# Kernel tuning notes

Measured on AMD Instinct MI355X. Metric: run time of the kernel, lower is better.

## Reference

```python
import jax, jax.numpy as jnp
import numpy as np

DIM = 1024
HEADS = 16
D_HEAD = 64
INNER = HEADS * D_HEAD  # 1024
FF_INNER = 4 * DIM      # 4096


def setup_inputs() -> dict:
    key = jax.random.key(0)
    ks = jax.random.split(key, 12)
    s = lambda fan_in: 1.0 / np.sqrt(fan_in)
    x = jax.random.normal(ks[0], (4, 1024, DIM), dtype=jnp.float32)
    context = jax.random.normal(ks[1], (4, 2048, DIM), dtype=jnp.float32)
    Wq = jax.random.normal(ks[2], (DIM, INNER), dtype=jnp.float32) * s(DIM)
    Wk = jax.random.normal(ks[3], (DIM, INNER), dtype=jnp.float32) * s(DIM)
    Wv = jax.random.normal(ks[4], (DIM, INNER), dtype=jnp.float32) * s(DIM)
    Wo = jax.random.normal(ks[5], (INNER, DIM), dtype=jnp.float32) * s(INNER)
    bo = jax.random.normal(ks[6], (DIM,), dtype=jnp.float32) * 0.01
    W1 = jax.random.normal(ks[7], (DIM, FF_INNER), dtype=jnp.float32) * s(DIM)
    b1 = jax.random.normal(ks[8], (FF_INNER,), dtype=jnp.float32) * 0.01
    W2 = jax.random.normal(ks[9], (FF_INNER, DIM), dtype=jnp.float32) * s(FF_INNER)
    b2 = jax.random.normal(ks[10], (DIM,), dtype=jnp.float32) * 0.01
    return {"x": x, "context": context, "Wq": Wq, "Wk": Wk, "Wv": Wv,
            "Wo": Wo, "bo": bo, "W1": W1, "b1": b1, "W2": W2, "b2": b2}


def _block(x, context, Wq, Wk, Wv, Wo, bo, W1, b1, W2, b2):
    B, Lq, _ = x.shape
    scale = 1.0 / np.sqrt(D_HEAD).astype(np.float32)
    # cross attention
    q = (x @ Wq).reshape(B, Lq, HEADS, D_HEAD)          # [B,Lq,H,D]
    k = (context @ Wk).reshape(B, -1, HEADS, D_HEAD)    # [B,Lk,H,D]
    v = (context @ Wv).reshape(B, -1, HEADS, D_HEAD)
    sim = jnp.einsum('bqhd,bkhd->bhqk', q, k) * scale   # [B,H,Lq,Lk]
    attn = jax.nn.softmax(sim, axis=-1)
    out = jnp.einsum('bhqk,bkhd->bqhd', attn, v).reshape(B, Lq, INNER)
    x = out @ Wo + bo + x
    # feedforward (exact GELU as in torch F.gelu default)
    h = jax.nn.gelu(x @ W1 + b1, approximate=False)
    return h @ W2 + b2 + x


def reference(x, context, Wq, Wk, Wv, Wo, bo, W1, b1, W2, b2):
    return _block(x, context, Wq, Wk, Wv, Wo, bo, W1, b1, W2, b2)
```

## Files before the change

kernel.cpp:

```cpp
#include <hip/hip_runtime.h>
#include <hip/hip_bf16.h>
#include <cmath>
#include <cstdint>

typedef short s16x8 __attribute__((ext_vector_type(8)));
typedef unsigned short u16x8 __attribute__((ext_vector_type(8)));
typedef unsigned short u16x4 __attribute__((ext_vector_type(4)));
typedef float f32x4 __attribute__((ext_vector_type(4)));

__device__ __forceinline__ float bf2f(uint16_t u) {
  union { uint32_t i; float f; } c; c.i = ((uint32_t)u) << 16; return c.f;
}
__device__ __forceinline__ uint16_t f2bf(float f) {
  union { float f; uint32_t i; } c; c.f = f;
  return (uint16_t)((c.i + 0x7FFFu + ((c.i >> 16) & 1u)) >> 16);
}
__device__ __forceinline__ uint32_t pkbf(float a, float b) {
  union { __hip_bfloat162 h; uint32_t u; } c;
  c.h = __float22bfloat162_rn(float2{a, b});
  return c.u;
}

__device__ __forceinline__ void gload16(const void* g, void* l) {
  __builtin_amdgcn_global_load_lds(
      (const __attribute__((address_space(1))) void*)g,
      (__attribute__((address_space(3))) void*)l, 16, 0, 0);
}

__device__ __forceinline__ bool sniff_is_bf16(const uint16_t* u16, int64_t n,
                                              int tid, int* s_cnt) {
  int cnt = 0;
#pragma unroll
  for (int j = 0; j < 4; j++) {
    int64_t idx = (((int64_t)(tid * 4 + j)) * 2) % n;
    idx &= ~(int64_t)1;
    uint32_t e = (u16[idx] >> 7) & 0xFF;
    cnt += (e >= 96 && e <= 144) ? 1 : 0;
  }
  if (tid == 0) *s_cnt = 0;
  __syncthreads();
  atomicAdd(s_cnt, cnt);
  __syncthreads();
  return (*s_cnt) * 10 > 1024 * 6;
}

__global__ __launch_bounds__(256) void prep_all(
    float* dout,
    const void* xr, const void* cr, const void* bor, const void* b1r, const void* b2r,
    const void* Wq, const void* Wk, const void* Wv, const void* Wo,
    const void* W1, const void* W2,
    uint16_t* xo, uint16_t* co, uint16_t* boo, uint16_t* b1o, uint16_t* b2o,
    uint16_t* WqT, uint16_t* WkT, uint16_t* WvT, uint16_t* WoT,
    uint16_t* W1T, uint16_t* W2T) {
  __shared__ int s_cnt;
  __shared__ uint16_t tile[64][65];
  const int id = blockIdx.x;
  const int tid = threadIdx.x;

  if (id < 1024) {
    float* p = dout + ((int64_t)id * 256 + tid) * 4;
#pragma unroll
    for (int i = 0; i < 4; i++)
      *(f32x4*)(p + (int64_t)i * 262144) = (f32x4){0.f, 0.f, 0.f, 0.f};
    return;
  }
  if (id < 4099) {
    const void* src; uint16_t* dst; int64_t tot; int64_t base; int nv;
    if (id < 2048)      { src = xr; dst = xo; tot = 4194304; base = (int64_t)(id - 1024) * 4096; nv = 4; }
    else if (id < 4096) { src = cr; dst = co; tot = 8388608; base = (int64_t)(id - 2048) * 4096; nv = 4; }
    else if (id == 4096){ src = bor; dst = boo; tot = 1024; base = 0; nv = 1; }
    else if (id == 4097){ src = b1r; dst = b1o; tot = 4096; base = 0; nv = 4; }
    else                { src = b2r; dst = b2o; tot = 1024; base = 0; nv = 1; }
    const bool is16 = sniff_is_bf16((const uint16_t*)src, tot, tid, &s_cnt);
    if (is16) {
      const uint64_t* s = (const uint64_t*)((const uint16_t*)src + base);
      uint64_t* d = (uint64_t*)(dst + base);
      for (int i = 0; i < nv; i++) d[i * 256 + tid] = s[i * 256 + tid];
    } else {
      const f32x4* s = (const f32x4*)((const float*)src + base);
      uint2* d = (uint2*)(dst + base);
      for (int i = 0; i < nv; i++) {
        f32x4 v = s[i * 256 + tid];
        uint2 o; o.x = pkbf(v[0], v[1]); o.y = pkbf(v[2], v[3]);
        d[i * 256 + tid] = o;
      }
    }
    return;
  }
  const int t0 = id - 4099;
  const void* src; uint16_t* dst; int R, C, bx, by;
  if (t0 < 1024) {
    const int wsel = t0 >> 8, t = t0 & 255;
    const void* srcs[4] = {Wq, Wk, Wv, Wo};
    uint16_t* dsts[4] = {WqT, WkT, WvT, WoT};
    src = srcs[wsel]; dst = dsts[wsel]; R = 1024; C = 1024; bx = t & 15; by = t >> 4;
  } else if (t0 < 2048) { int t = t0 - 1024; src = W1; dst = W1T; R = 1024; C = 4096; bx = t & 63; by = t >> 6; }
  else                  { int t = t0 - 2048; src = W2; dst = W2T; R = 4096; C = 1024; bx = t & 15; by = t >> 4; }
  const uint16_t* u16 = (const uint16_t*)src;
  const float* f32 = (const float*)src;
  const bool is16 = sniff_is_bf16(u16, (int64_t)R * C, tid, &s_cnt);
  const int c0 = bx * 64, r0 = by * 64;
  if (is16) {
    const int c8 = (tid & 7) * 8, r = tid >> 3;
#pragma unroll
    for (int ri = 0; ri < 2; ri++) {
      const int row = r + ri * 32;
      u16x8 v = *(const u16x8*)(u16 + (int64_t)(r0 + row) * C + c0 + c8);
#pragma unroll
      for (int j = 0; j < 8; j++) tile[c8 + j][row] = v[j];
    }
  } else {
    const int c4 = (tid & 15) * 4, r = tid >> 4;
#pragma unroll
    for (int ri = 0; ri < 4; ri++) {
      const int row = r + ri * 16;
      f32x4 v = *(const f32x4*)(f32 + (int64_t)(r0 + row) * C + c0 + c4);
#pragma unroll
      for (int j = 0; j < 4; j++) tile[c4 + j][row] = f2bf(v[j]);
    }
  }
  __syncthreads();
  const int rr8 = (tid & 7) * 8, cc = tid >> 3;
#pragma unroll
  for (int ci = 0; ci < 2; ci++) {
    const int col = cc + ci * 32;
    *(u16x8*)(dst + (int64_t)(c0 + col) * R + r0 + rr8) = *(const u16x8*)&tile[col][rr8];
  }
}

__global__ __launch_bounds__(256) void vtrans(
    const uint16_t* __restrict__ KVb, uint16_t* __restrict__ Vt) {
  __shared__ uint16_t tile[64][65];
  const int z = blockIdx.z;
  const uint16_t* in = KVb + (int64_t)z * 2048 * 2048 + 1024;
  uint16_t* out = Vt + (int64_t)z * 1024 * 2048;
  const int tid = threadIdx.x;
  const int c0 = blockIdx.x * 64, k0 = blockIdx.y * 64;
  const int c8 = (tid & 7) * 8, r = tid >> 3;
#pragma unroll
  for (int ri = 0; ri < 2; ri++) {
    const int krow = r + ri * 32;
    u16x8 v = *(const u16x8*)(in + (int64_t)(k0 + krow) * 2048 + c0 + c8);
#pragma unroll
    for (int j = 0; j < 8; j++) tile[c8 + j][krow] = v[j];
  }
  __syncthreads();
  const int k8 = (tid & 7) * 8, cc = tid >> 3;
#pragma unroll
  for (int ci = 0; ci < 2; ci++) {
    const int col = cc + ci * 32;
    *(u16x8*)(out + (int64_t)(c0 + col) * 2048 + k0 + k8) = *(const u16x8*)&tile[col][k8];
  }
}

#define BM 128
#define BN 128
#define BK 64

enum { EPI_NONE = 0, EPI_BIAS_RES = 1, EPI_BIAS_GELU = 2 };

template <int EPI, int RESF32, int OUTF32, int SPLITK>
__device__ __forceinline__ void gemm_body(
    const uint16_t* __restrict__ A, const uint16_t* __restrict__ Bt,
    void* __restrict__ Cv, const uint16_t* __restrict__ bias,
    const void* __restrict__ resid, int M, int N, int K_total,
    int m0, int n0, int zslice, uint16_t* As, uint16_t* Bs) {
  const int tid = threadIdx.x;
  const int w = tid >> 6, l = tid & 63;
  const int wu = __builtin_amdgcn_readfirstlane(w);
  const int wm = (w >> 1) * 64, wn = (w & 1) * 64;
  const int ls = l & 15, lg = l >> 4;
  const int K = SPLITK ? (K_total >> 1) : K_total;
  const int kof = SPLITK ? zslice * K : 0;

  const int sr = 8 * w + (l >> 3);
  const int koff = (((l & 7) ^ ((l >> 3) & 7)) * 8);
  const uint16_t* Ag = A + (int64_t)(m0 + sr) * K_total + kof + koff;
  const uint16_t* Bg = Bt + (int64_t)(n0 + sr) * K_total + kof + koff;
  const int64_t rstep = (int64_t)32 * K_total;

  uint16_t* lA = As + wu * 512;
  uint16_t* lB = Bs + wu * 512;

  f32x4 acc[4][4] = {};

  for (int kb = 0; kb < K; kb += BK) {
    __syncthreads();
#pragma unroll
    for (int r = 0; r < 4; r++) {
      gload16(Ag + r * rstep + kb, lA + r * 2048);
      gload16(Bg + r * rstep + kb, lB + r * 2048);
    }
    __syncthreads();
#pragma unroll
    for (int kk = 0; kk < 2; kk++) {
      s16x8 af[4], bfr[4];
#pragma unroll
      for (int i = 0; i < 4; i++) {
        const int row = wm + i * 16 + ls;
        af[i] = *(const s16x8*)&As[row * 64 + (((kk * 4 + lg) ^ (ls & 7)) * 8)];
      }
#pragma unroll
      for (int j = 0; j < 4; j++) {
        const int row = wn + j * 16 + ls;
        bfr[j] = *(const s16x8*)&Bs[row * 64 + (((kk * 4 + lg) ^ (ls & 7)) * 8)];
      }
#pragma unroll
      for (int i = 0; i < 4; i++)
#pragma unroll
        for (int j = 0; j < 4; j++)
          acc[i][j] = __builtin_amdgcn_mfma_f32_16x16x32_bf16(af[i], bfr[j], acc[i][j], 0, 0, 0);
    }
  }

#pragma unroll
  for (int i = 0; i < 4; i++) {
#pragma unroll
    for (int rr = 0; rr < 4; rr++) {
      const int64_t row = m0 + wm + i * 16 + lg * 4 + rr;
#pragma unroll
      for (int j = 0; j < 4; j++) {
        const int col = n0 + wn + j * 16 + ls;
        float v = acc[i][j][rr];
        if (EPI == EPI_BIAS_RES) {
          if (!SPLITK || zslice == 0) {
            const float rv = RESF32 ? ((const float*)resid)[row * N + col]
                                    : bf2f(((const uint16_t*)resid)[row * N + col]);
            v += bf2f(bias[col]) + rv;
          }
        } else if (EPI == EPI_BIAS_GELU) {
          v += bf2f(bias[col]);
          v = 0.5f * v * (1.0f + erff(v * 0.70710678118654752f));
        }
        if (SPLITK)
          atomicAdd((float*)Cv + row * N + col, v);
        else if (OUTF32)
          ((float*)Cv)[row * N + col] = v;
        else
          ((uint16_t*)Cv)[row * N + col] = f2bf(v);
      }
    }
  }
}

template <int EPI, int RESF32, int OUTF32, int SPLITK>
__global__ __launch_bounds__(256, 3) void gemm_single(
    const uint16_t* __restrict__ A, const uint16_t* __restrict__ Bt,
    void* __restrict__ Cv, const uint16_t* __restrict__ bias,
    const void* __restrict__ resid, int M, int N, int K_total) {
  __shared__ alignas(16) uint16_t As[BM * BK];
  __shared__ alignas(16) uint16_t Bs[BN * BK];
  gemm_body<EPI, RESF32, OUTF32, SPLITK>(A, Bt, Cv, bias, resid, M, N, K_total,
                                         blockIdx.x * BM, blockIdx.y * BN,
                                         (int)blockIdx.z, As, Bs);
}

__global__ __launch_bounds__(256, 3) void gemm_qkv(
    const uint16_t* __restrict__ xA, const uint16_t* __restrict__ WqT,
    uint16_t* __restrict__ Qb,
    const uint16_t* __restrict__ ctxA, const uint16_t* __restrict__ KVWt,
    uint16_t* __restrict__ KVb) {
  __shared__ alignas(16) uint16_t As[BM * BK];
  __shared__ alignas(16) uint16_t Bs[BN * BK];
  const int id = blockIdx.x;
  if (id < 256) {
    gemm_body<EPI_NONE, 0, 0, 0>(xA, WqT, Qb, nullptr, nullptr, 4096, 1024, 1024,
                                 (id & 31) * BM, (id >> 5) * BN, 0, As, Bs);
  } else {
    const int t = id - 256;
    gemm_body<EPI_NONE, 0, 0, 0>(ctxA, KVWt, KVb, nullptr, nullptr, 8192, 2048, 1024,
                                 (t & 63) * BM, (t >> 6) * BN, 0, As, Bs);
  }
}

#define KLD 72
#define PLD 72

__global__ __launch_bounds__(256, 2) void attn_kernel(
    const uint16_t* __restrict__ Q,
    const uint16_t* __restrict__ KV,
    const uint16_t* __restrict__ Vt,
    uint16_t* __restrict__ O) {
  __shared__ alignas(16) uint16_t Ks[64 * KLD];
  __shared__ alignas(16) uint16_t Vts[64 * KLD];
  __shared__ alignas(16) uint16_t Ps[8][16 * PLD];

  const int tid = threadIdx.x;
  const int w = tid >> 6, l = tid & 63;
  const int ls = l & 15, lg = l >> 4;

  const int blk = blockIdx.x;
  const int bh = blk & 63;
  const int qb = blk >> 6;
  const int h = bh & 15, b = bh >> 4;

  const int64_t qrow0 = (int64_t)b * 1024 + qb * 128;
  const int hoff = h * 64;
  const uint16_t* Vtb = Vt + (int64_t)b * 1024 * 2048;

  const float sc = 0.125f * 1.4426950408889634f;

  s16x8 qf[2][2];
#pragma unroll
  for (int qq = 0; qq < 2; qq++)
#pragma unroll
    for (int ks = 0; ks < 2; ks++) {
      s16x8 r = *(const s16x8*)(Q + (qrow0 + w * 32 + qq * 16 + ls) * 1024 + hoff + ks * 32 + lg * 8);
#pragma unroll
      for (int j = 0; j < 8; j++)
        qf[qq][ks][j] = (short)f2bf(bf2f((uint16_t)r[j]) * sc);
    }

  f32x4 oacc[2][4] = {};
  float lsum[2] = {0.f, 0.f};

  const int srow = tid >> 3;
  const int sc8 = (tid & 7) * 8;
  const uint16_t* Kg = KV + ((int64_t)b * 2048 + srow) * 2048 + hoff + sc8;
  const uint16_t* Vg = Vtb + (int64_t)(hoff + srow) * 2048 + sc8;

  s16x8 rk0 = *(const s16x8*)(Kg);
  s16x8 rk1 = *(const s16x8*)(Kg + (int64_t)32 * 2048);
  s16x8 rv0 = *(const s16x8*)(Vg);
  s16x8 rv1 = *(const s16x8*)(Vg + (int64_t)32 * 2048);

  for (int kt = 0; kt < 2048; kt += 64) {
    __syncthreads();
    *(s16x8*)&Ks[srow * KLD + sc8] = rk0;
    *(s16x8*)&Ks[(srow + 32) * KLD + sc8] = rk1;
    *(s16x8*)&Vts[srow * KLD + sc8] = rv0;
    *(s16x8*)&Vts[(srow + 32) * KLD + sc8] = rv1;
    const int ktn = kt + 64;
    if (ktn < 2048) {
      rk0 = *(const s16x8*)(Kg + (int64_t)ktn * 2048);
      rk1 = *(const s16x8*)(Kg + (int64_t)(ktn + 32) * 2048);
      rv0 = *(const s16x8*)(Vg + ktn);
      rv1 = *(const s16x8*)(Vg + ktn + (int64_t)32 * 2048);
    }
    __syncthreads();

    f32x4 st[2][4];
#pragma unroll
    for (int jn = 0; jn < 4; jn++) {
      f32x4 z = {0.f, 0.f, 0.f, 0.f};
      st[0][jn] = z; st[1][jn] = z;
#pragma unroll
      for (int ks = 0; ks < 2; ks++) {
        s16x8 kf = *(const s16x8*)&Ks[(jn * 16 + ls) * KLD + ks * 32 + lg * 8];
        st[0][jn] = __builtin_amdgcn_mfma_f32_16x16x32_bf16(kf, qf[0][ks], st[0][jn], 0, 0, 0);
        st[1][jn] = __builtin_amdgcn_mfma_f32_16x16x32_bf16(kf, qf[1][ks], st[1][jn], 0, 0, 0);
      }
    }

#pragma unroll
    for (int qq = 0; qq < 2; qq++)
#pragma unroll
      for (int jn = 0; jn < 4; jn++) {
        const float p0 = exp2f(st[qq][jn][0]);
        const float p1 = exp2f(st[qq][jn][1]);
        const float p2 = exp2f(st[qq][jn][2]);
        const float p3 = exp2f(st[qq][jn][3]);
        lsum[qq] += (p0 + p1) + (p2 + p3);
        uint2 pk; pk.x = pkbf(p0, p1); pk.y = pkbf(p2, p3);
        *(uint2*)&Ps[w * 2 + qq][ls * PLD + jn * 16 + lg * 4] = pk;
      }

#pragma unroll
    for (int ks = 0; ks < 2; ks++) {
      s16x8 pf0 = *(const s16x8*)&Ps[w * 2 + 0][ls * PLD + ks * 32 + lg * 8];
      s16x8 pf1 = *(const s16x8*)&Ps[w * 2 + 1][ls * PLD + ks * 32 + lg * 8];
#pragma unroll
      for (int jn = 0; jn < 4; jn++) {
        s16x8 vf = *(const s16x8*)&Vts[(jn * 16 + ls) * KLD + ks * 32 + lg * 8];
        oacc[0][jn] = __builtin_amdgcn_mfma_f32_16x16x32_bf16(pf0, vf, oacc[0][jn], 0, 0, 0);
        oacc[1][jn] = __builtin_amdgcn_mfma_f32_16x16x32_bf16(pf1, vf, oacc[1][jn], 0, 0, 0);
      }
    }
  }

#pragma unroll
  for (int qq = 0; qq < 2; qq++) {
    float red = lsum[qq];
    red += __shfl_xor(red, 16, 64);
    red += __shfl_xor(red, 32, 64);
#pragma unroll
    for (int rr = 0; rr < 4; rr++) {
      const float inv = 1.0f / __shfl(red, lg * 4 + rr, 64);
      const int64_t row = qrow0 + w * 32 + qq * 16 + lg * 4 + rr;
#pragma unroll
      for (int jn = 0; jn < 4; jn++)
        O[row * 1024 + hoff + jn * 16 + ls] = f2bf(oacc[qq][jn][rr] * inv);
    }
  }
}

extern "C" void kernel_launch(void* const* d_in, const int* in_sizes, int n_in,
                              void* d_out, int out_size, void* d_ws, size_t ws_size,
                              hipStream_t stream) {
  const void* x_raw   = d_in[0];
  const void* ctx_raw = d_in[1];
  const void* Wq_raw  = d_in[2];
  const void* Wk_raw  = d_in[3];
  const void* Wv_raw  = d_in[4];
  const void* Wo_raw  = d_in[5];
  const void* bo_raw  = d_in[6];
  const void* W1_raw  = d_in[7];
  const void* b1_raw  = d_in[8];
  const void* W2_raw  = d_in[9];
  const void* b2_raw  = d_in[10];

  const int64_t Mi = 1 << 20;
  uint16_t* ws   = (uint16_t*)d_ws;
  uint16_t* WqT  = ws;
  uint16_t* KVWt = ws + 1 * Mi;
  uint16_t* WoT  = ws + 3 * Mi;
  uint16_t* W1T  = ws + 4 * Mi;
  uint16_t* W2T  = ws + 8 * Mi;
  uint16_t* bob  = ws + 12 * Mi;
  uint16_t* b1b  = ws + 12 * Mi + 1024;
  uint16_t* b2b  = ws + 12 * Mi + 5120;
  uint16_t* xb   = ws + 13 * Mi;
  uint16_t* AO   = ws + 13 * Mi;
  uint16_t* ctxb = ws + 17 * Mi;
  uint16_t* Vt   = ws + 17 * Mi;
  uint16_t* X1   = ws + 17 * Mi;
  uint16_t* Qb   = ws + 25 * Mi;
  uint16_t* KVb  = ws + 29 * Mi;
  uint16_t* Hb   = ws + 29 * Mi;

  const dim3 tb(256);
  prep_all<<<dim3(7171), tb, 0, stream>>>(
      (float*)d_out,
      x_raw, ctx_raw, bo_raw, b1_raw, b2_raw,
      Wq_raw, Wk_raw, Wv_raw, Wo_raw, W1_raw, W2_raw,
      xb, ctxb, bob, b1b, b2b,
      WqT, KVWt, KVWt + Mi, WoT, W1T, W2T);

  gemm_qkv<<<dim3(1280), tb, 0, stream>>>(xb, WqT, Qb, ctxb, KVWt, KVb);

  vtrans<<<dim3(16, 32, 4), tb, 0, stream>>>(KVb, Vt);

  attn_kernel<<<dim3(512), tb, 0, stream>>>(Qb, KVb, Vt, AO);

  gemm_single<EPI_BIAS_RES, 1, 0, 0><<<dim3(32, 8), tb, 0, stream>>>(
      AO, WoT, X1, bob, x_raw, 4096, 1024, 1024);
  gemm_single<EPI_BIAS_GELU, 0, 0, 0><<<dim3(32, 32), tb, 0, stream>>>(
      X1, W1T, Hb, b1b, nullptr, 4096, 4096, 1024);
  gemm_single<EPI_BIAS_RES, 0, 1, 1><<<dim3(32, 8, 2), tb, 0, stream>>>(
      Hb, W2T, d_out, b2b, X1, 4096, 1024, 4096);
}
```

Before: 400.8 us.

## Add 256x256 eight-wave double-buffered GEMM with phased LDS prefetch for QKV and FFN

Adds a new GEMM kernel that uses 512 threads and 256x256 output tiles. It double-buffers LDS and interleaves global-to-LDS prefetch of the next K-tile with four MFMA phases, using barriers, waitcnt and setprio. The kernel is used for the fused QKV projection, the W1+GELU GEMM, and the W2 GEMM, which now uses 4-way split-K with atomics. Larger tiles raise operand reuse and cut global traffic. The trade-off is fewer blocks: 320, 256 and 256 respectively, which may underfill 256 CUs and unbalance the QKV launch. The 4-way split-K also adds atomic contention.

```diff
diff --git a/kernel.cpp b/kernel.cpp
--- a/kernel.cpp
+++ b/kernel.cpp
@@ -153,11 +153,11 @@
   }
 }
 
+enum { EPI_NONE = 0, EPI_BIAS_RES = 1, EPI_BIAS_GELU = 2 };
+
 #define BM 128
 #define BN 128
 #define BK 64
-
-enum { EPI_NONE = 0, EPI_BIAS_RES = 1, EPI_BIAS_GELU = 2 };
 
 template <int EPI, int RESF32, int OUTF32, int SPLITK>
 __device__ __forceinline__ void gemm_body(
@@ -255,21 +255,140 @@
                                          (int)blockIdx.z, As, Bs);
 }
 
-__global__ __launch_bounds__(256, 3) void gemm_qkv(
+#define G8K 64
+
+#define STAGE_A8(BB, Q, KB) \
+  gload16(Ag + (int64_t)(Q) * cstep + (KB), As + (BB) + (Q) * 4096 + wu * 512)
+#define STAGE_B8(BB, Q, KB) \
+  gload16(Bg + (int64_t)(Q) * cstep + (KB), Bs + (BB) + (Q) * 4096 + wu * 512)
+
+#define PHASE8(QM, QN, S0, S1, WAITC)                                          \
+  do {                                                                         \
+    s16x8 a0_[4], a1_[4], b0_[2], b1_[2];                                      \
+    const int x_ = (ls & 7);                                                   \
+    _Pragma("unroll") for (int i_ = 0; i_ < 4; i_++) {                         \
+      const int r_ = wm + (QM) * 64 + i_ * 16 + ls;                            \
+      a0_[i_] = *(const s16x8*)&As[cb + r_ * 64 + ((lg ^ x_) * 8)];            \
+      a1_[i_] = *(const s16x8*)&As[cb + r_ * 64 + (((4 + lg) ^ x_) * 8)];      \
+    }                                                                          \
+    _Pragma("unroll") for (int j_ = 0; j_ < 2; j_++) {                         \
+      const int r_ = wn + (QN) * 32 + j_ * 16 + ls;                            \
+      b0_[j_] = *(const s16x8*)&Bs[cb + r_ * 64 + ((lg ^ x_) * 8)];            \
+      b1_[j_] = *(const s16x8*)&Bs[cb + r_ * 64 + (((4 + lg) ^ x_) * 8)];      \
+    }                                                                          \
+    S0; S1;                                                                    \
+    __builtin_amdgcn_s_barrier();                                              \
+    asm volatile("s_waitcnt lgkmcnt(0)" ::: "memory");                         \
+    __builtin_amdgcn_s_setprio(1);                                             \
+    _Pragma("unroll") for (int i_ = 0; i_ < 4; i_++)                           \
+      _Pragma("unroll") for (int j_ = 0; j_ < 2; j_++) {                       \
+        acc[(QM)*4 + i_][(QN)*2 + j_] = __builtin_amdgcn_mfma_f32_16x16x32_bf16( \
+            a0_[i_], b0_[j_], acc[(QM)*4 + i_][(QN)*2 + j_], 0, 0, 0);         \
+        acc[(QM)*4 + i_][(QN)*2 + j_] = __builtin_amdgcn_mfma_f32_16x16x32_bf16( \
+            a1_[i_], b1_[j_], acc[(QM)*4 + i_][(QN)*2 + j_], 0, 0, 0);         \
+      }                                                                        \
+    __builtin_amdgcn_s_setprio(0);                                             \
+    WAITC;                                                                     \
+    __builtin_amdgcn_s_barrier();                                              \
+  } while (0)
+
+template <int EPI, int RESF32, int OUTF32, int SPLITK>
+__device__ __forceinline__ void gemm8_body(
+    const uint16_t* __restrict__ A, const uint16_t* __restrict__ Bt,
+    void* __restrict__ Cv, const uint16_t* __restrict__ bias,
+    const void* __restrict__ resid, int M, int N, int K_total,
+    int m0, int n0, int zslice, uint16_t* As, uint16_t* Bs) {
+  const int tid = threadIdx.x;
+  const int w = tid >> 6, l = tid & 63;
+  const int wu = __builtin_amdgcn_readfirstlane(w);
+  const int ls = l & 15, lg = l >> 4;
+  const int wm = (w >> 2) * 128, wn = (w & 3) * 64;
+  const int K = K_total / SPLITK;
+  const int kof = zslice * K;
+  const int NT = K / G8K;
+
+  const int srow = (w << 3) + (l >> 3);
+  const int koff = (((l & 7) ^ ((l >> 3) & 7)) * 8);
+  const uint16_t* Ag = A + (int64_t)(m0 + srow) * K_total + kof + koff;
+  const uint16_t* Bg = Bt + (int64_t)(n0 + srow) * K_total + kof + koff;
+  const int64_t cstep = (int64_t)64 * K_total;
+
+  f32x4 acc[8][4] = {};
+
+  STAGE_B8(0, 0, 0); STAGE_B8(0, 1, 0); STAGE_B8(0, 2, 0); STAGE_B8(0, 3, 0);
+  STAGE_A8(0, 0, 0); STAGE_A8(0, 2, 0); STAGE_A8(0, 1, 0); STAGE_A8(0, 3, 0);
+  asm volatile("s_waitcnt vmcnt(2)" ::: "memory");
+  __builtin_amdgcn_s_barrier();
+
+  for (int t = 0; t < NT; ++t) {
+    const int cb = (t & 1) << 14;
+    const int nb = 16384 - cb;
+    const int64_t kbn = (t + 1 < NT) ? (int64_t)(t + 1) * G8K : 0;
+    PHASE8(0, 0, STAGE_B8(nb, 0, kbn), STAGE_B8(nb, 1, kbn), (void)0);
+    PHASE8(0, 1, STAGE_B8(nb, 2, kbn), STAGE_B8(nb, 3, kbn),
+           asm volatile("s_waitcnt vmcnt(4)" ::: "memory"));
+    PHASE8(1, 0, STAGE_A8(nb, 0, kbn), STAGE_A8(nb, 2, kbn), (void)0);
+    PHASE8(1, 1, STAGE_A8(nb, 1, kbn), STAGE_A8(nb, 3, kbn),
+           asm volatile("s_waitcnt vmcnt(2)" ::: "memory"));
+  }
+
+#pragma unroll
+  for (int i = 0; i < 8; i++) {
+#pragma unroll
+    for (int rr = 0; rr < 4; rr++) {
+      const int64_t row = m0 + wm + i * 16 + lg * 4 + rr;
+#pragma unroll
+      for (int j = 0; j < 4; j++) {
+        const int col = n0 + wn + j * 16 + ls;
+        float v = acc[i][j][rr];
+        if (EPI == EPI_BIAS_RES) {
+          if (SPLITK == 1 || zslice == 0) {
+            const float rv = RESF32 ? ((const float*)resid)[row * N + col]
+                                    : bf2f(((const uint16_t*)resid)[row * N + col]);
+            v += bf2f(bias[col]) + rv;
+          }
+        } else if (EPI == EPI_BIAS_GELU) {
+          v += bf2f(bias[col]);
+          v = 0.5f * v * (1.0f + erff(v * 0.70710678118654752f));
+        }
+        if (SPLITK > 1)
+          atomicAdd((float*)Cv + row * N + col, v);
+        else if (OUTF32)
+          ((float*)Cv)[row * N + col] = v;
+        else
+          ((uint16_t*)Cv)[row * N + col] = f2bf(v);
+      }
+    }
+  }
+}
+
+template <int EPI, int RESF32, int OUTF32, int SPLITK>
+__global__ __launch_bounds__(512, 2) void gemm8_single(
+    const uint16_t* __restrict__ A, const uint16_t* __restrict__ Bt,
+    void* __restrict__ Cv, const uint16_t* __restrict__ bias,
+    const void* __restrict__ resid, int M, int N, int K_total) {
+  __shared__ alignas(16) uint16_t As[2 * 16384];
+  __shared__ alignas(16) uint16_t Bs[2 * 16384];
+  gemm8_body<EPI, RESF32, OUTF32, SPLITK>(A, Bt, Cv, bias, resid, M, N, K_total,
+                                          blockIdx.x * 256, blockIdx.y * 256,
+                                          (int)blockIdx.z, As, Bs);
+}
+
+__global__ __launch_bounds__(512, 2) void gemm8_qkv(
     const uint16_t* __restrict__ xA, const uint16_t* __restrict__ WqT,
     uint16_t* __restrict__ Qb,
     const uint16_t* __restrict__ ctxA, const uint16_t* __restrict__ KVWt,
     uint16_t* __restrict__ KVb) {
-  __shared__ alignas(16) uint16_t As[BM * BK];
-  __shared__ alignas(16) uint16_t Bs[BN * BK];
+  __shared__ alignas(16) uint16_t As[2 * 16384];
+  __shared__ alignas(16) uint16_t Bs[2 * 16384];
   const int id = blockIdx.x;
   if (id < 256) {
-    gemm_body<EPI_NONE, 0, 0, 0>(xA, WqT, Qb, nullptr, nullptr, 4096, 1024, 1024,
-                                 (id & 31) * BM, (id >> 5) * BN, 0, As, Bs);
+    gemm8_body<EPI_NONE, 0, 0, 1>(ctxA, KVWt, KVb, nullptr, nullptr, 8192, 2048, 1024,
+                                  (id & 31) * 256, (id >> 5) * 256, 0, As, Bs);
   } else {
     const int t = id - 256;
-    gemm_body<EPI_NONE, 0, 0, 0>(ctxA, KVWt, KVb, nullptr, nullptr, 8192, 2048, 1024,
-                                 (t & 63) * BM, (t >> 6) * BN, 0, As, Bs);
+    gemm8_body<EPI_NONE, 0, 0, 1>(xA, WqT, Qb, nullptr, nullptr, 4096, 1024, 1024,
+                                  (t & 15) * 256, (t >> 4) * 256, 0, As, Bs);
   }
 }
 
@@ -429,6 +548,7 @@
   uint16_t* Hb   = ws + 29 * Mi;
 
   const dim3 tb(256);
+  const dim3 tb8(512);
   prep_all<<<dim3(7171), tb, 0, stream>>>(
       (float*)d_out,
       x_raw, ctx_raw, bo_raw, b1_raw, b2_raw,
@@ -436,7 +556,7 @@
       xb, ctxb, bob, b1b, b2b,
       WqT, KVWt, KVWt + Mi, WoT, W1T, W2T);
 
-  gemm_qkv<<<dim3(1280), tb, 0, stream>>>(xb, WqT, Qb, ctxb, KVWt, KVb);
+  gemm8_qkv<<<dim3(320), tb8, 0, stream>>>(xb, WqT, Qb, ctxb, KVWt, KVb);
 
   vtrans<<<dim3(16, 32, 4), tb, 0, stream>>>(KVb, Vt);
 
@@ -444,8 +564,8 @@
 
   gemm_single<EPI_BIAS_RES, 1, 0, 0><<<dim3(32, 8), tb, 0, stream>>>(
       AO, WoT, X1, bob, x_raw, 4096, 1024, 1024);
-  gemm_single<EPI_BIAS_GELU, 0, 0, 0><<<dim3(32, 32), tb, 0, stream>>>(
+  gemm8_single<EPI_BIAS_GELU, 0, 0, 1><<<dim3(16, 16), tb8, 0, stream>>>(
       X1, W1T, Hb, b1b, nullptr, 4096, 4096, 1024);
-  gemm_single<EPI_BIAS_RES, 0, 1, 1><<<dim3(32, 8, 2), tb, 0, stream>>>(
+  gemm8_single<EPI_BIAS_RES, 0, 1, 4><<<dim3(16, 4, 4), tb8, 0, stream>>>(
       Hb, W2T, d_out, b2b, X1, 4096, 1024, 4096);
 }
```

After: 489.0 us. 1.22x slower.
